# Optimization experiments

Hardware: AMD Instinct MI355X
Metric: run time of the kernel (lower is better)

## Reference

```python
import jax, jax.numpy as jnp
import numpy as np

N, L, H, E = 2, 2048, 8, 64
S = 2048
C_CLUSTERS = 256
ITERATIONS = 10
BITS = 32
TOPK = 32


def setup_inputs() -> dict:
    key = jax.random.key(0)
    k1, k2, k3, k4 = jax.random.split(key, 4)
    return {
        "queries": jax.random.normal(k1, (N, L, H, E), dtype=jnp.float32),
        "keys": jax.random.normal(k2, (N, S, H, E), dtype=jnp.float32),
        "values": jax.random.normal(k3, (N, S, H, E), dtype=jnp.float32),
        "planes": jax.random.normal(k4, (BITS, E + 1), dtype=jnp.float32),
    }


def _hash_bits(Q, planes):
    # Q: [N,H,L,E]; planes: [B, E+1] (last column is the hash bias)
    proj = jnp.einsum('nhle,be->nhlb', Q, planes[:, :-1]) + planes[:, -1]
    return (proj > 0).astype(jnp.float32)  # [N,H,L,B]


def _kmeans_hamming(hbits, n_clusters, iterations):
    # Lloyd iterations with hamming distance on the hash bit-vectors.
    n, h, l, b = hbits.shape
    init_idx = (jnp.arange(n_clusters) * l) // n_clusters
    cent = hbits[:, :, init_idx, :]  # [N,H,C,B], bits in {0,1}
    hsum = hbits.sum(-1)  # [N,H,L]

    def assign(cent):
        csum = cent.sum(-1)  # [N,H,C]
        # hamming(h,c) = sum_b h + sum_b c - 2 h.c for binary vectors
        dist = hsum[..., None] + csum[:, :, None, :] \
            - 2.0 * jnp.einsum('nhlb,nhcb->nhlc', hbits, cent)
        return jnp.argmin(dist, axis=-1)  # [N,H,L]

    def body(cent, _):
        a = assign(cent)
        oh = jax.nn.one_hot(a, n_clusters, dtype=jnp.float32)  # [N,H,L,C]
        counts = oh.sum(2)  # [N,H,C]
        sums = jnp.einsum('nhlc,nhlb->nhcb', oh, hbits)
        new = (sums / jnp.maximum(counts, 1.0)[..., None] >= 0.5).astype(jnp.float32)
        cent = jnp.where(counts[..., None] > 0, new, cent)  # keep empty centroids
        return cent, None

    cent, _ = jax.lax.scan(body, cent, None, length=iterations)
    a = assign(cent)
    oh = jax.nn.one_hot(a, n_clusters, dtype=jnp.float32)
    counts = oh.sum(2)
    return a, counts, oh


def reference(queries, keys, values, planes):
    Q = jnp.transpose(queries, (0, 2, 1, 3))  # [N,H,L,E]
    K = jnp.transpose(keys, (0, 2, 1, 3))     # [N,H,S,E]
    V = jnp.transpose(values, (0, 2, 1, 3))   # [N,H,S,E]
    n, h, l, e = Q.shape
    t = 1.0 / jnp.sqrt(jnp.asarray(e, jnp.float32))

    # --- hash & cluster queries (non-differentiable routing) ---
    hbits = _hash_bits(jax.lax.stop_gradient(Q), planes)
    clusters, counts, oh = _kmeans_hamming(hbits, C_CLUSTERS, ITERATIONS)

    # --- group queries: per-cluster mean (=_GroupQueries) ---
    safe = jnp.maximum(counts, 1.0)
    Qg = jnp.einsum('nhlc,nhle->nhce', oh, Q) / safe[..., None]  # [N,H,C,E]

    QK = jnp.einsum('nhce,nhse->nhcs', Qg, K)  # [N,H,C,S]; key mask is all zeros
    topv, topi = jax.lax.top_k(QK, TOPK)       # [N,H,C,k]

    # --- bottom-k attention (full softmax with top-k zeroed) ---
    A = jax.nn.softmax(t * QK, axis=-1)
    n_i = jnp.arange(n)[:, None, None, None]
    h_i = jnp.arange(h)[None, :, None, None]
    c_i = jnp.arange(C_CLUSTERS)[None, None, :, None]
    A_masked = A.at[n_i, h_i, c_i, topi].set(0.0)
    A_bk = A_masked.sum(-1)  # [N,H,C]
    Vg = jnp.einsum('nhcs,nhse->nhce', A_masked, V)  # [N,H,C,E]
    V_bottom = jnp.take_along_axis(Vg, clusters[..., None], axis=2)  # broadcast -> [N,H,L,E]
    A_bk_q = jnp.take_along_axis(A_bk, clusters, axis=2)  # [N,H,L]

    # --- top-k attention recomputed per query with its cluster's top-k keys ---
    top_q = jnp.take_along_axis(topi, clusters[..., None], axis=2)  # [N,H,L,k]
    idx = top_q.reshape(n, h, l * TOPK)[..., None]
    Kq = jnp.take_along_axis(K, idx, axis=2).reshape(n, h, l, TOPK, e)
    QKt = jnp.einsum('nhle,nhlke->nhlk', Q, Kq)
    At = jax.nn.softmax(t * QKt, axis=-1) * (1.0 - A_bk_q)[..., None]
    Vq = jnp.take_along_axis(V, idx, axis=2).reshape(n, h, l, TOPK, e)
    V_top = jnp.einsum('nhlk,nhlke->nhle', At, Vq)

    out = V_top + V_bottom  # [N,H,L,E]
    return jnp.transpose(out, (0, 2, 1, 3))  # [N,L,H,E]
```

## Files before the change

### kernel.cpp

```cpp
#include <hip/hip_runtime.h>
#include <math.h>
#include <float.h>

#define NB 2
#define LQ 2048
#define HH 8
#define EE 64
#define SS 2048
#define CC 256
#define KM_ITERS 10
#define NBITS 32
#define TK 32
#define NH (NB*HH)
#define CG 4

__global__ __launch_bounds__(256) void k_hash(const float* __restrict__ Q,
                                              const float* __restrict__ planes,
                                              unsigned int* __restrict__ qmask) {
    int gid = blockIdx.x * 256 + threadIdx.x;
    int nh = gid >> 11, l = gid & (LQ - 1);
    int n = nh >> 3, h = nh & 7;
    const float* qrow = Q + (((size_t)n * LQ + l) * HH + h) * EE;
    float q[64];
    #pragma unroll
    for (int e = 0; e < 64; e++) q[e] = qrow[e];
    unsigned int m = 0;
    for (int b = 0; b < NBITS; b++) {
        double acc = (double)planes[b * 65 + 64];
        #pragma unroll
        for (int e = 0; e < 64; e++) acc += (double)q[e] * (double)planes[b * 65 + e];
        if (acc > 0.0) m |= (1u << b);
    }
    qmask[gid] = m;
}

__global__ __launch_bounds__(256) void k_cinit(const unsigned int* __restrict__ qmask,
                                               unsigned int* __restrict__ cent_g) {
    int nh = blockIdx.x, t = threadIdx.x;
    cent_g[nh * CC + t] = qmask[(size_t)nh * LQ + t * 8];
}

__global__ __launch_bounds__(256) void k_assign(const unsigned int* __restrict__ qmask,
                                                const unsigned int* __restrict__ cent_g,
                                                int* __restrict__ asg) {
    int nh = blockIdx.x >> 3;
    int p = ((blockIdx.x & 7) << 8) + threadIdx.x;
    int t = threadIdx.x;
    __shared__ __align__(16) unsigned int cent[CC];
    cent[t] = cent_g[nh * CC + t];
    __syncthreads();
    unsigned int m = qmask[(size_t)nh * LQ + p];
    int best = 0x7fffffff;
    const uint4* c4p = (const uint4*)cent;
    #pragma unroll 4
    for (int c4 = 0; c4 < CC / 4; c4++) {
        uint4 cm = c4p[c4];
        int base = c4 << 2;
        int e0 = (__popc(m ^ cm.x) << 8) + base;
        int e1 = (__popc(m ^ cm.y) << 8) + base + 1;
        int e2 = (__popc(m ^ cm.z) << 8) + base + 2;
        int e3 = (__popc(m ^ cm.w) << 8) + base + 3;
        int e01 = e0 < e1 ? e0 : e1;
        int e23 = e2 < e3 ? e2 : e3;
        int e = e01 < e23 ? e01 : e23;
        best = best < e ? best : e;
    }
    asg[(size_t)nh * LQ + p] = best & 255;
}

__global__ __launch_bounds__(512) void k_update(const unsigned int* __restrict__ qmask,
                                                const int* __restrict__ asg,
                                                unsigned int* __restrict__ cent_g) {
    int nh = blockIdx.x, t = threadIdx.x;
    __shared__ unsigned int sorted[LQ];
    __shared__ int cnts[CC], offs[CC], cursor[CC];
    if (t < CC) cnts[t] = 0;
    int bc[4]; unsigned int mym[4];
    #pragma unroll
    for (int k = 0; k < 4; k++) {
        bc[k] = asg[(size_t)nh * LQ + t + k * 512];
        mym[k] = qmask[(size_t)nh * LQ + t + k * 512];
    }
    __syncthreads();
    #pragma unroll
    for (int k = 0; k < 4; k++) atomicAdd(&cnts[bc[k]], 1);
    __syncthreads();
    if (t < 64) {
        int c0 = cnts[4 * t], c1 = cnts[4 * t + 1], c2 = cnts[4 * t + 2], c3 = cnts[4 * t + 3];
        int s1 = c0 + c1, s2 = s1 + c2, tot = s2 + c3;
        int inc = tot;
        #pragma unroll
        for (int o = 1; o < 64; o <<= 1) {
            int v = __shfl_up(inc, o);
            if (t >= o) inc += v;
        }
        int excl = inc - tot;
        offs[4 * t] = excl;          cursor[4 * t] = excl;
        offs[4 * t + 1] = excl + c0; cursor[4 * t + 1] = excl + c0;
        offs[4 * t + 2] = excl + s1; cursor[4 * t + 2] = excl + s1;
        offs[4 * t + 3] = excl + s2; cursor[4 * t + 3] = excl + s2;
    }
    __syncthreads();
    int cl = t >> 1, j = t & 1;
    int cnt_c = cnts[cl], off_c = offs[cl];
    #pragma unroll
    for (int k = 0; k < 4; k++) {
        int pos = atomicAdd(&cursor[bc[k]], 1);
        sorted[pos] = mym[k];
    }
    __syncthreads();
    int bs[32];
    #pragma unroll
    for (int b = 0; b < 32; b++) bs[b] = 0;
    for (int i = j; i < cnt_c; i += 2) {
        unsigned int m = sorted[off_c + i];
        #pragma unroll
        for (int b = 0; b < 32; b++) bs[b] += (m >> b) & 1;
    }
    #pragma unroll
    for (int b = 0; b < 32; b++) bs[b] += __shfl_xor(bs[b], 1);
    if (j == 0 && cnt_c > 0) {
        unsigned int nc = 0;
        #pragma unroll
        for (int b = 0; b < 32; b++) if (2 * bs[b] >= cnt_c) nc |= (1u << b);
        cent_g[nh * CC + cl] = nc;
    }
}

__global__ __launch_bounds__(512) void k_finalize(const int* __restrict__ asg,
                                                  int* __restrict__ counts_out,
                                                  int* __restrict__ order_out,
                                                  int* __restrict__ offsets_out) {
    int nh = blockIdx.x, t = threadIdx.x;
    __shared__ int cnts[CC], offs[CC], cursor[CC];
    if (t < CC) cnts[t] = 0;
    int bc[4];
    #pragma unroll
    for (int k = 0; k < 4; k++) bc[k] = asg[(size_t)nh * LQ + t + k * 512];
    __syncthreads();
    #pragma unroll
    for (int k = 0; k < 4; k++) atomicAdd(&cnts[bc[k]], 1);
    __syncthreads();
    if (t < 64) {
        int c0 = cnts[4 * t], c1 = cnts[4 * t + 1], c2 = cnts[4 * t + 2], c3 = cnts[4 * t + 3];
        int s1 = c0 + c1, s2 = s1 + c2, tot = s2 + c3;
        int inc = tot;
        #pragma unroll
        for (int o = 1; o < 64; o <<= 1) {
            int v = __shfl_up(inc, o);
            if (t >= o) inc += v;
        }
        int excl = inc - tot;
        offs[4 * t] = excl;          cursor[4 * t] = excl;
        offs[4 * t + 1] = excl + c0; cursor[4 * t + 1] = excl + c0;
        offs[4 * t + 2] = excl + s1; cursor[4 * t + 2] = excl + s1;
        offs[4 * t + 3] = excl + s2; cursor[4 * t + 3] = excl + s2;
    }
    __syncthreads();
    if (t < CC) {
        counts_out[nh * CC + t] = cnts[t];
        offsets_out[nh * CC + t] = offs[t];
    }
    #pragma unroll
    for (int k = 0; k < 4; k++) {
        int pos = atomicAdd(&cursor[bc[k]], 1);
        order_out[(size_t)nh * LQ + pos] = t + k * 512;
    }
}

__global__ __launch_bounds__(256) void k_qg(const float* __restrict__ Q,
                                            const int* __restrict__ order,
                                            const int* __restrict__ offsets,
                                            const int* __restrict__ counts,
                                            double* __restrict__ Qg) {
    int nh = blockIdx.x >> 6;
    int c = (blockIdx.x & 63) * 4 + (threadIdx.x >> 6);
    int e = threadIdx.x & 63;
    int n = nh >> 3, h = nh & 7;
    int off = offsets[nh * CC + c];
    int cnt = counts[nh * CC + c];
    const int* ord = order + (size_t)nh * LQ + off;
    double acc = 0.0;
    for (int i = 0; i < cnt; i++) {
        int p = ord[i];
        acc += (double)Q[(((size_t)n * LQ + p) * HH + h) * EE + e];
    }
    double safe = cnt > 0 ? (double)cnt : 1.0;
    Qg[((size_t)(nh * CC + c)) * EE + e] = acc / safe;
}

__global__ __launch_bounds__(256) void k_transpose(const float* __restrict__ Kp,
                                                   float* __restrict__ Kt) {
    int nh = blockIdx.x >> 5;
    int s0 = (blockIdx.x & 31) * 64;
    int n = nh >> 3, h = nh & 7;
    __shared__ float tile[64][65];
    int t = threadIdx.x;
    int e = t & 63, r0 = t >> 6;
    #pragma unroll
    for (int j = 0; j < 16; j++) {
        int r = r0 * 16 + j;
        tile[r][e] = Kp[(((size_t)n * SS + s0 + r) * HH + h) * EE + e];
    }
    __syncthreads();
    int sl = t & 63, eg = t >> 6;
    #pragma unroll
    for (int j = 0; j < 16; j++) {
        int ee_ = eg * 16 + j;
        Kt[((size_t)nh * EE + ee_) * SS + s0 + sl] = tile[sl][ee_];
    }
}

__global__ __launch_bounds__(256) void k_rows(const float* __restrict__ Kt,
                                              const float* __restrict__ Vp,
                                              const double* __restrict__ Qg,
                                              int* __restrict__ topi,
                                              float* __restrict__ abk,
                                              float* __restrict__ Vg) {
    int bid = blockIdx.x;
    int xcd = bid & 7, idx = bid >> 3;
    int nh = xcd * 2 + (idx >> 6);
    int cg = idx & 63;
    int c0 = cg * CG;
    int n = nh >> 3, h = nh & 7;
    int t = threadIdx.x, w = t >> 6, l = t & 63;

    __shared__ double qgl[EE][CG];
    __shared__ double xrowc[CG][512];
    float* wbuf = (float*)&xrowc[0][0];
    float* redv = (float*)&xrowc[2][0];

    qgl[t >> 2][t & 3] = Qg[((size_t)(nh * CC + c0 + (t & 3))) * EE + (t >> 2)];
    __syncthreads();

    double acc[8][CG];
    #pragma unroll
    for (int r = 0; r < 8; r++)
        #pragma unroll
        for (int c = 0; c < CG; c++) acc[r][c] = 0.0;
    const float* ktb = Kt + ((size_t)nh * EE) * SS + t;
    for (int e = 0; e < EE; e++) {
        double q0 = qgl[e][0], q1 = qgl[e][1], q2 = qgl[e][2], q3 = qgl[e][3];
        const float* kr = ktb + (size_t)e * SS;
        #pragma unroll
        for (int r = 0; r < 8; r++) {
            double kv = (double)kr[r * 256];
            acc[r][0] += q0 * kv; acc[r][1] += q1 * kv;
            acc[r][2] += q2 * kv; acc[r][3] += q3 * kv;
        }
    }

    double v[32];
    #pragma unroll
    for (int j = 0; j < 4; j++) {
        __syncthreads();
        #pragma unroll
        for (int c = 0; c < CG; c++) {
            xrowc[c][t]       = acc[2 * j][c];
            xrowc[c][256 + t] = acc[2 * j + 1][c];
        }
        __syncthreads();
        #pragma unroll
        for (int m = 0; m < 8; m++)
            v[8 * j + m] = xrowc[w][((m >> 2) << 8) + ((m & 3) << 6) + l];
    }

    double m = v[0];
    #pragma unroll
    for (int k = 1; k < 32; k++) m = v[k] > m ? v[k] : m;
    #pragma unroll
    for (int o = 32; o > 0; o >>= 1) { double z = __shfl_xor(m, o); m = z > m ? z : m; }

    double ds = 0.0;
    #pragma unroll
    for (int k = 0; k < 32; k++) ds += (double)expf(0.125f * (float)(v[k] - m));
    #pragma unroll
    for (int o = 32; o > 0; o >>= 1) ds += __shfl_xor(ds, o);

    unsigned ext = 0;
    double lbv = -1e301; int lbi = 1 << 30;
    #pragma unroll
    for (int k = 0; k < 32; k++)
        if (v[k] > lbv) { lbv = v[k]; lbi = l + k * 64; }
    double topsum = 0.0;
    int rowid = nh * CC + c0 + w;
    for (int kk = 0; kk < TK; kk++) {
        double bv = lbv; int bi = lbi;
        #pragma unroll
        for (int o = 32; o > 0; o >>= 1) {
            double v2 = __shfl_xor(bv, o); int i2 = __shfl_xor(bi, o);
            if (v2 > bv || (v2 == bv && i2 < bi)) { bv = v2; bi = i2; }
        }
        topsum += (double)expf(0.125f * (float)(bv - m));
        if (l == 0) topi[(size_t)rowid * TK + kk] = bi;
        if ((bi & 63) == l) {
            ext |= 1u << (bi >> 6);
            lbv = -1e301; lbi = 1 << 30;
            #pragma unroll
            for (int k = 0; k < 32; k++)
                if (!((ext >> k) & 1) && v[k] > lbv) { lbv = v[k]; lbi = l + k * 64; }
        }
    }
    if (l == 0) abk[rowid] = (float)((ds - topsum) / ds);

    float invd = (float)(1.0 / ds);
    float w32r[32];
    #pragma unroll
    for (int k = 0; k < 32; k++)
        w32r[k] = ((ext >> k) & 1) ? 0.0f
                : expf(0.125f * (float)(v[k] - m)) * invd;

    float a0 = 0.f, a1 = 0.f, a2 = 0.f, a3 = 0.f;
    const float* vb = Vp + (((size_t)n * SS) * HH + h) * EE + l;
    #pragma unroll
    for (int j = 0; j < 4; j++) {
        __syncthreads();
        #pragma unroll
        for (int m2 = 0; m2 < 8; m2++)
            wbuf[(((m2 << 6) + l) << 2) + w] = w32r[8 * j + m2];
        __syncthreads();
        const float4* wp4 = (const float4*)wbuf;
        int sbase = 512 * j + 128 * w;
        for (int s = 0; s < 128; s++) {
            float4 wv = wp4[128 * w + s];
            float vv = vb[(size_t)(sbase + s) * HH * EE];
            a0 += wv.x * vv; a1 += wv.y * vv; a2 += wv.z * vv; a3 += wv.w * vv;
        }
    }
    {
        int e = l, grp = w;
        redv[(grp * 4 + 0) * 64 + e] = a0;
        redv[(grp * 4 + 1) * 64 + e] = a1;
        redv[(grp * 4 + 2) * 64 + e] = a2;
        redv[(grp * 4 + 3) * 64 + e] = a3;
        __syncthreads();
        int c = w;
        float s = redv[(0 * 4 + c) * 64 + e] + redv[(1 * 4 + c) * 64 + e]
                + redv[(2 * 4 + c) * 64 + e] + redv[(3 * 4 + c) * 64 + e];
        Vg[((size_t)(nh * CC + c0 + c)) * EE + e] = s;
    }
}

__global__ __launch_bounds__(256) void k_out(const float* __restrict__ Q,
                                             const float* __restrict__ Kp,
                                             const float* __restrict__ Vp,
                                             const int* __restrict__ clusters,
                                             const int* __restrict__ topi,
                                             const float* __restrict__ abk,
                                             const float* __restrict__ Vg,
                                             float* __restrict__ out) {
    int tid = threadIdx.x, wid = tid >> 6, e = tid & 63;
    int q = blockIdx.x * 4 + wid;
    int nh = q >> 11, l = q & (LQ - 1);
    int n = nh >> 3, h = nh & 7;
    int c = clusters[q];
    float scale = 1.0f - abk[nh * CC + c];
    const int* ti = topi + (size_t)(nh * CC + c) * TK;
    float qe = Q[(((size_t)n * LQ + l) * HH + h) * EE + e];
    float myv = -INFINITY;
    for (int k = 0; k < TK; k++) {
        int idx = ti[k];
        float kv = Kp[(((size_t)n * SS + idx) * HH + h) * EE + e];
        float v = qe * kv;
        #pragma unroll
        for (int o = 32; o > 0; o >>= 1) v += __shfl_xor(v, o);
        if (e == k) myv = v;
    }
    float mv = myv;
    #pragma unroll
    for (int o = 32; o > 0; o >>= 1) { float v = __shfl_xor(mv, o); mv = v > mv ? v : mv; }
    float p = (e < TK) ? expf(0.125f * (myv - mv)) : 0.0f;
    float ssum = p;
    #pragma unroll
    for (int o = 32; o > 0; o >>= 1) ssum += __shfl_xor(ssum, o);
    float at = p / ssum * scale;
    float acc = 0.0f;
    for (int k = 0; k < TK; k++) {
        float wk = __shfl(at, k, 64);
        int idx = ti[k];
        acc += wk * Vp[(((size_t)n * SS + idx) * HH + h) * EE + e];
    }
    acc += Vg[(size_t)(nh * CC + c) * EE + e];
    out[(((size_t)n * LQ + l) * HH + h) * EE + e] = acc;
}

extern "C" void kernel_launch(void* const* d_in, const int* in_sizes, int n_in,
                              void* d_out, int out_size, void* d_ws, size_t ws_size,
                              hipStream_t stream) {
    const float* Q      = (const float*)d_in[0];
    const float* K      = (const float*)d_in[1];
    const float* V      = (const float*)d_in[2];
    const float* planes = (const float*)d_in[3];
    float* out = (float*)d_out;

    char* ws = (char*)d_ws;
    unsigned int* qmask    = (unsigned int*)(ws);
    int*          clusters = (int*)(ws + (128 << 10));
    int*          counts   = (int*)(ws + (256 << 10));
    float*        abk      = (float*)(ws + (272 << 10));
    int*          topi     = (int*)(ws + (288 << 10));
    float*        Vg       = (float*)(ws + (800 << 10));
    double*       Qg       = (double*)(ws + (1824 << 10));
    float*        Kt       = (float*)(ws + (4096 << 10));
    int*          order    = (int*)(ws + (12288 << 10));
    int*          offsets  = (int*)(ws + (12416 << 10));
    unsigned int* cent_g   = (unsigned int*)(ws + (12432 << 10));

    k_transpose<<<dim3(NH * 32), dim3(256), 0, stream>>>(K, Kt);
    k_hash<<<dim3(NH * LQ / 256), dim3(256), 0, stream>>>(Q, planes, qmask);
    k_cinit<<<dim3(NH), dim3(256), 0, stream>>>(qmask, cent_g);
    for (int it = 0; it < KM_ITERS; ++it) {
        k_assign<<<dim3(NH * 8), dim3(256), 0, stream>>>(qmask, cent_g, clusters);
        k_update<<<dim3(NH), dim3(512), 0, stream>>>(qmask, clusters, cent_g);
    }
    k_assign<<<dim3(NH * 8), dim3(256), 0, stream>>>(qmask, cent_g, clusters);
    k_finalize<<<dim3(NH), dim3(512), 0, stream>>>(clusters, counts, order, offsets);
    k_qg<<<dim3(NH * 64), dim3(256), 0, stream>>>(Q, order, offsets, counts, Qg);
    k_rows<<<dim3(NH * CC / CG), dim3(256), 0, stream>>>(Kt, V, Qg, topi, abk, Vg);
    k_out<<<dim3(NH * LQ / 4), dim3(256), 0, stream>>>(Q, K, V, clusters, topi, abk, Vg, out);
}
```

Before: 421.4 us.

## Fuse k-means init, assign, update and finalize into one persistent block per head

Replaces the init kernel, the 11 assign launches, the 10 update launches and the finalize kernel with a single 1024-thread block per (n,h). That block keeps centroids in shared memory across all Lloyd iterations. This removes about 22 launches and the global round trips for centroids and assignments. The cost is that only 16 blocks run, so the assign phase, which used to run on 128 blocks, now runs with far less parallelism across the GPU.

New measurement: 534.1 us. +26.7%, slower.

```diff
diff --git a/kernel.cpp b/kernel.cpp
--- a/kernel.cpp
+++ b/kernel.cpp
@@ -34,56 +34,98 @@
     qmask[gid] = m;
 }
 
-__global__ __launch_bounds__(256) void k_cinit(const unsigned int* __restrict__ qmask,
-                                               unsigned int* __restrict__ cent_g) {
-    int nh = blockIdx.x, t = threadIdx.x;
-    cent_g[nh * CC + t] = qmask[(size_t)nh * LQ + t * 8];
-}
-
-__global__ __launch_bounds__(256) void k_assign(const unsigned int* __restrict__ qmask,
-                                                const unsigned int* __restrict__ cent_g,
-                                                int* __restrict__ asg) {
-    int nh = blockIdx.x >> 3;
-    int p = ((blockIdx.x & 7) << 8) + threadIdx.x;
+__global__ __launch_bounds__(1024) void k_kmeans_mono(const unsigned int* __restrict__ qmask,
+                                                      int* __restrict__ clusters,
+                                                      int* __restrict__ counts_out,
+                                                      int* __restrict__ order_out,
+                                                      int* __restrict__ offsets_out) {
+    int nh = blockIdx.x;
     int t = threadIdx.x;
     __shared__ __align__(16) unsigned int cent[CC];
-    cent[t] = cent_g[nh * CC + t];
-    __syncthreads();
-    unsigned int m = qmask[(size_t)nh * LQ + p];
-    int best = 0x7fffffff;
-    const uint4* c4p = (const uint4*)cent;
-    #pragma unroll 4
-    for (int c4 = 0; c4 < CC / 4; c4++) {
-        uint4 cm = c4p[c4];
-        int base = c4 << 2;
-        int e0 = (__popc(m ^ cm.x) << 8) + base;
-        int e1 = (__popc(m ^ cm.y) << 8) + base + 1;
-        int e2 = (__popc(m ^ cm.z) << 8) + base + 2;
-        int e3 = (__popc(m ^ cm.w) << 8) + base + 3;
-        int e01 = e0 < e1 ? e0 : e1;
-        int e23 = e2 < e3 ? e2 : e3;
-        int e = e01 < e23 ? e01 : e23;
-        best = best < e ? best : e;
-    }
-    asg[(size_t)nh * LQ + p] = best & 255;
-}
-
-__global__ __launch_bounds__(512) void k_update(const unsigned int* __restrict__ qmask,
-                                                const int* __restrict__ asg,
-                                                unsigned int* __restrict__ cent_g) {
-    int nh = blockIdx.x, t = threadIdx.x;
-    __shared__ unsigned int sorted[LQ];
+    __shared__ unsigned int sortedm[LQ];
     __shared__ int cnts[CC], offs[CC], cursor[CC];
+
+    const unsigned int* qb = qmask + (size_t)nh * LQ;
+    unsigned int m0 = qb[t], m1 = qb[t + 1024];
+    if (t < CC) cent[t] = qb[t * 8];
+    __syncthreads();
+
+    int bc0 = 0, bc1 = 0;
+    for (int it = 0; it <= KM_ITERS; ++it) {
+        int b0 = 0x7fffffff, b1 = 0x7fffffff;
+        const uint4* c4p = (const uint4*)cent;
+        #pragma unroll 4
+        for (int c4 = 0; c4 < CC / 4; c4++) {
+            uint4 cm = c4p[c4];
+            int base = c4 << 2;
+            int e;
+            e = (__popc(m0 ^ cm.x) << 8) + base;     b0 = b0 < e ? b0 : e;
+            e = (__popc(m0 ^ cm.y) << 8) + base + 1; b0 = b0 < e ? b0 : e;
+            e = (__popc(m0 ^ cm.z) << 8) + base + 2; b0 = b0 < e ? b0 : e;
+            e = (__popc(m0 ^ cm.w) << 8) + base + 3; b0 = b0 < e ? b0 : e;
+            e = (__popc(m1 ^ cm.x) << 8) + base;     b1 = b1 < e ? b1 : e;
+            e = (__popc(m1 ^ cm.y) << 8) + base + 1; b1 = b1 < e ? b1 : e;
+            e = (__popc(m1 ^ cm.z) << 8) + base + 2; b1 = b1 < e ? b1 : e;
+            e = (__popc(m1 ^ cm.w) << 8) + base + 3; b1 = b1 < e ? b1 : e;
+        }
+        bc0 = b0 & 255; bc1 = b1 & 255;
+        if (it == KM_ITERS) break;
+
+        __syncthreads();
+        if (t < CC) cnts[t] = 0;
+        __syncthreads();
+        atomicAdd(&cnts[bc0], 1); atomicAdd(&cnts[bc1], 1);
+        __syncthreads();
+        if (t < 64) {
+            int c0 = cnts[4 * t], c1 = cnts[4 * t + 1], c2 = cnts[4 * t + 2], c3 = cnts[4 * t + 3];
+            int s1 = c0 + c1, s2 = s1 + c2, tot = s2 + c3;
+            int inc = tot;
+            #pragma unroll
+            for (int o = 1; o < 64; o <<= 1) {
+                int v = __shfl_up(inc, o);
+                if (t >= o) inc += v;
+            }
+            int excl = inc - tot;
+            offs[4 * t] = excl;          cursor[4 * t] = excl;
+            offs[4 * t + 1] = excl + c0; cursor[4 * t + 1] = excl + c0;
+            offs[4 * t + 2] = excl + s1; cursor[4 * t + 2] = excl + s1;
+            offs[4 * t + 3] = excl + s2; cursor[4 * t + 3] = excl + s2;
+        }
+        __syncthreads();
+        { int p0 = atomicAdd(&cursor[bc0], 1); sortedm[p0] = m0; }
+        { int p1 = atomicAdd(&cursor[bc1], 1); sortedm[p1] = m1; }
+        __syncthreads();
+
+        int c = t >> 2, slot = t & 3;
+        int cnt_c = cnts[c], off_c = offs[c];
+        int bs[32];
+        #pragma unroll
+        for (int b = 0; b < 32; b++) bs[b] = 0;
+        for (int i = slot; i < cnt_c; i += 4) {
+            unsigned int mm = sortedm[off_c + i];
+            #pragma unroll
+            for (int b = 0; b < 32; b++) bs[b] += (mm >> b) & 1;
+        }
+        #pragma unroll
+        for (int b = 0; b < 32; b++) {
+            bs[b] += __shfl_xor(bs[b], 1);
+            bs[b] += __shfl_xor(bs[b], 2);
+        }
+        if (slot == 0 && cnt_c > 0) {
+            unsigned int nc = 0;
+            #pragma unroll
+            for (int b = 0; b < 32; b++) if (2 * bs[b] >= cnt_c) nc |= (1u << b);
+            cent[c] = nc;
+        }
+        __syncthreads();
+    }
+
+    clusters[(size_t)nh * LQ + t] = bc0;
+    clusters[(size_t)nh * LQ + t + 1024] = bc1;
+    __syncthreads();
     if (t < CC) cnts[t] = 0;
-    int bc[4]; unsigned int mym[4];
-    #pragma unroll
-    for (int k = 0; k < 4; k++) {
-        bc[k] = asg[(size_t)nh * LQ + t + k * 512];
-        mym[k] = qmask[(size_t)nh * LQ + t + k * 512];
-    }
-    __syncthreads();
-    #pragma unroll
-    for (int k = 0; k < 4; k++) atomicAdd(&cnts[bc[k]], 1);
+    __syncthreads();
+    atomicAdd(&cnts[bc0], 1); atomicAdd(&cnts[bc1], 1);
     __syncthreads();
     if (t < 64) {
         int c0 = cnts[4 * t], c1 = cnts[4 * t + 1], c2 = cnts[4 * t + 2], c3 = cnts[4 * t + 3];
@@ -101,71 +143,12 @@
         offs[4 * t + 3] = excl + s2; cursor[4 * t + 3] = excl + s2;
     }
     __syncthreads();
-    int cl = t >> 1, j = t & 1;
-    int cnt_c = cnts[cl], off_c = offs[cl];
-    #pragma unroll
-    for (int k = 0; k < 4; k++) {
-        int pos = atomicAdd(&cursor[bc[k]], 1);
-        sorted[pos] = mym[k];
-    }
-    __syncthreads();
-    int bs[32];
-    #pragma unroll
-    for (int b = 0; b < 32; b++) bs[b] = 0;
-    for (int i = j; i < cnt_c; i += 2) {
-        unsigned int m = sorted[off_c + i];
-        #pragma unroll
-        for (int b = 0; b < 32; b++) bs[b] += (m >> b) & 1;
-    }
-    #pragma unroll
-    for (int b = 0; b < 32; b++) bs[b] += __shfl_xor(bs[b], 1);
-    if (j == 0 && cnt_c > 0) {
-        unsigned int nc = 0;
-        #pragma unroll
-        for (int b = 0; b < 32; b++) if (2 * bs[b] >= cnt_c) nc |= (1u << b);
-        cent_g[nh * CC + cl] = nc;
-    }
-}
-
-__global__ __launch_bounds__(512) void k_finalize(const int* __restrict__ asg,
-                                                  int* __restrict__ counts_out,
-                                                  int* __restrict__ order_out,
-                                                  int* __restrict__ offsets_out) {
-    int nh = blockIdx.x, t = threadIdx.x;
-    __shared__ int cnts[CC], offs[CC], cursor[CC];
-    if (t < CC) cnts[t] = 0;
-    int bc[4];
-    #pragma unroll
-    for (int k = 0; k < 4; k++) bc[k] = asg[(size_t)nh * LQ + t + k * 512];
-    __syncthreads();
-    #pragma unroll
-    for (int k = 0; k < 4; k++) atomicAdd(&cnts[bc[k]], 1);
-    __syncthreads();
-    if (t < 64) {
-        int c0 = cnts[4 * t], c1 = cnts[4 * t + 1], c2 = cnts[4 * t + 2], c3 = cnts[4 * t + 3];
-        int s1 = c0 + c1, s2 = s1 + c2, tot = s2 + c3;
-        int inc = tot;
-        #pragma unroll
-        for (int o = 1; o < 64; o <<= 1) {
-            int v = __shfl_up(inc, o);
-            if (t >= o) inc += v;
-        }
-        int excl = inc - tot;
-        offs[4 * t] = excl;          cursor[4 * t] = excl;
-        offs[4 * t + 1] = excl + c0; cursor[4 * t + 1] = excl + c0;
-        offs[4 * t + 2] = excl + s1; cursor[4 * t + 2] = excl + s1;
-        offs[4 * t + 3] = excl + s2; cursor[4 * t + 3] = excl + s2;
-    }
-    __syncthreads();
     if (t < CC) {
         counts_out[nh * CC + t] = cnts[t];
         offsets_out[nh * CC + t] = offs[t];
     }
-    #pragma unroll
-    for (int k = 0; k < 4; k++) {
-        int pos = atomicAdd(&cursor[bc[k]], 1);
-        order_out[(size_t)nh * LQ + pos] = t + k * 512;
-    }
+    { int p0 = atomicAdd(&cursor[bc0], 1); order_out[(size_t)nh * LQ + p0] = t; }
+    { int p1 = atomicAdd(&cursor[bc1], 1); order_out[(size_t)nh * LQ + p1] = t + 1024; }
 }
 
 __global__ __launch_bounds__(256) void k_qg(const float* __restrict__ Q,
@@ -404,17 +387,10 @@
     float*        Kt       = (float*)(ws + (4096 << 10));
     int*          order    = (int*)(ws + (12288 << 10));
     int*          offsets  = (int*)(ws + (12416 << 10));
-    unsigned int* cent_g   = (unsigned int*)(ws + (12432 << 10));
 
     k_transpose<<<dim3(NH * 32), dim3(256), 0, stream>>>(K, Kt);
     k_hash<<<dim3(NH * LQ / 256), dim3(256), 0, stream>>>(Q, planes, qmask);
-    k_cinit<<<dim3(NH), dim3(256), 0, stream>>>(qmask, cent_g);
-    for (int it = 0; it < KM_ITERS; ++it) {
-        k_assign<<<dim3(NH * 8), dim3(256), 0, stream>>>(qmask, cent_g, clusters);
-        k_update<<<dim3(NH), dim3(512), 0, stream>>>(qmask, clusters, cent_g);
-    }
-    k_assign<<<dim3(NH * 8), dim3(256), 0, stream>>>(qmask, cent_g, clusters);
-    k_finalize<<<dim3(NH), dim3(512), 0, stream>>>(clusters, counts, order, offsets);
+    k_kmeans_mono<<<dim3(NH), dim3(1024), 0, stream>>>(qmask, clusters, counts, order, offsets);
     k_qg<<<dim3(NH * 64), dim3(256), 0, stream>>>(Q, order, offsets, counts, Qg);
     k_rows<<<dim3(NH * CC / CG), dim3(256), 0, stream>>>(Kt, V, Qg, topi, abk, Vg);
     k_out<<<dim3(NH * LQ / 4), dim3(256), 0, stream>>>(Q, K, V, clusters, topi, abk, Vg, out);
```
